# Optimization experiments

Hardware: AMD Instinct MI355X
Metric: run time of the kernel (lower is better)

The kernel has to match this reference:

```python
import jax, jax.numpy as jnp
import numpy as np

B, L, D, H = 4, 2048, 512, 8
HD = D // H  # 64
MAX_REL = 4


def setup_inputs() -> dict:
    key = jax.random.key(0)
    ks = jax.random.split(key, 13)
    s = 1.0 / np.sqrt(D)
    return {
        "q": jax.random.normal(ks[0], (B, L, D), jnp.float32),
        "k": jax.random.normal(ks[1], (B, L, D), jnp.float32),
        "v": jax.random.normal(ks[2], (B, L, D), jnp.float32),
        "Wq": jax.random.normal(ks[3], (D, D), jnp.float32) * s,
        "bq": jax.random.normal(ks[4], (D,), jnp.float32) * 0.01,
        "Wk": jax.random.normal(ks[5], (D, D), jnp.float32) * s,
        "bk": jax.random.normal(ks[6], (D,), jnp.float32) * 0.01,
        "Wv": jax.random.normal(ks[7], (D, D), jnp.float32) * s,
        "bv": jax.random.normal(ks[8], (D,), jnp.float32) * 0.01,
        "Wo": jax.random.normal(ks[9], (D, D), jnp.float32) * s,
        "bo": jax.random.normal(ks[10], (D,), jnp.float32) * 0.01,
        "rel_k_table": jax.random.normal(ks[11], (2 * MAX_REL + 1, HD), jnp.float32),
        "rel_v_table": jax.random.normal(ks[12], (2 * MAX_REL + 1, HD), jnp.float32),
    }


def _to_heads(x):
    # [B, L, D] -> [B, H, L, HD]
    b, l, d = x.shape
    return x.reshape(b, l, H, d // H).transpose(0, 2, 1, 3)


def reference(q, k, v, Wq, bq, Wk, bk, Wv, bv, Wo, bo, rel_k_table, rel_v_table):
    # NOTE: in the source, the relative-attention output is overwritten by the
    # plain SDPA call immediately after, so observable math = SDPA only.
    # rel_k_table / rel_v_table are dead parameters (zero gradient).
    relu = jax.nn.relu
    qh = _to_heads(relu(q @ Wq.T + bq))  # [B,H,L,HD]
    kh = _to_heads(relu(k @ Wk.T + bk))
    vh = _to_heads(relu(v @ Wv.T + bv))
    # scale by sqrt(d_key)=sqrt(512), matching the original (not sqrt(head_dim))
    scores = jnp.einsum("bhqd,bhkd->bhqk", qh, kh) / jnp.sqrt(jnp.float32(D))
    attn = jax.nn.softmax(scores, axis=-1)
    out = jnp.einsum("bhqk,bhkd->bhqd", attn, vh)  # [B,H,L,HD]
    out = out.transpose(0, 2, 1, 3).reshape(B, L, D)
    return relu(out @ Wo.T + bo)
```

## Files before the change

### kernel.cpp

```cpp
#include <hip/hip_runtime.h>
#include <hip/hip_bf16.h>

#define B_  4
#define L_  2048
#define D_  512
#define H_  8
#define HD_ 64
#define M_  (B_ * L_)

typedef __bf16 bf16;
typedef __attribute__((ext_vector_type(8)))  __bf16 bf16x8;
typedef __attribute__((ext_vector_type(4)))  __bf16 bf16x4;
typedef __attribute__((ext_vector_type(16))) float  f32x16;

__device__ __forceinline__ f32x16 mfma32(bf16x8 a, bf16x8 b, f32x16 c) {
    return __builtin_amdgcn_mfma_f32_32x32x16_bf16(a, b, c, 0, 0, 0);
}

__device__ __forceinline__ void pack_body(const float* __restrict__ src,
                                          bf16* __restrict__ dst, int R,
                                          int m0, int k0)
{
    __shared__ __align__(16) bf16 tile[64][76];
    const int t = threadIdx.x;
#pragma unroll
    for (int rep = 0; rep < 4; rep++) {
        const int idx = rep * 256 + t;
        const int r = idx >> 4, c4 = idx & 15;
        const float4 f = *(const float4*)(src + (size_t)(m0 + r) * 512 + k0 + c4 * 4);
        bf16x4 v; v[0] = (bf16)f.x; v[1] = (bf16)f.y; v[2] = (bf16)f.z; v[3] = (bf16)f.w;
        *(bf16x4*)(&tile[r][c4 * 4]) = v;
    }
    __syncthreads();
#pragma unroll
    for (int rep = 0; rep < 2; rep++) {
        const int s = rep * 256 + t;
        const int ml = s & 63, kpl = s >> 6;
        const bf16x4 lo = *(const bf16x4*)(&tile[ml][kpl * 8]);
        const bf16x4 hi4 = *(const bf16x4*)(&tile[ml][kpl * 8 + 4]);
        bf16x8 v;
#pragma unroll
        for (int e = 0; e < 4; e++) { v[e] = lo[e]; v[e + 4] = hi4[e]; }
        *(bf16x8*)(dst + ((size_t)(k0 / 8 + kpl) * R + m0 + ml) * 8) = v;
    }
}

__global__ __launch_bounds__(256) void pack_all(
    const float* __restrict__ q, const float* __restrict__ k,
    const float* __restrict__ v,
    const float* __restrict__ W0, const float* __restrict__ W1,
    const float* __restrict__ W2, const float* __restrict__ W3,
    bf16* __restrict__ Wp, bf16* __restrict__ P0, bf16* __restrict__ P1,
    bf16* __restrict__ P2)
{
    const int z = blockIdx.z;
    if (z < 4) {
        if (blockIdx.x >= 8) return;
        const float* src = z == 0 ? W0 : z == 1 ? W1 : z == 2 ? W2 : W3;
        pack_body(src, Wp + (size_t)z * 64 * 512 * 8, 512, blockIdx.x * 64, blockIdx.y * 64);
    } else {
        const float* src = z == 4 ? q : z == 5 ? k : v;
        bf16* dst = z == 4 ? P0 : z == 5 ? P1 : P2;
        pack_body(src, dst, M_, blockIdx.x * 64, blockIdx.y * 64);
    }
}

struct PJob {
    const bf16* X; const bf16* W; const float* bias; void* out;
    float postmul; int mode;
};

__global__ __launch_bounds__(256, 3) void proj_kernel(PJob j0, PJob j1, PJob j2)
{
    const PJob jb = (blockIdx.z == 0) ? j0 : (blockIdx.z == 1) ? j1 : j2;
    const int w    = threadIdx.x >> 6;
    const int lane = threadIdx.x & 63;
    const int l31  = lane & 31;
    const int hi   = lane >> 5;
    const int m0 = blockIdx.x * 128;
    const int n0 = blockIdx.y * 128;
    const int mh = w & 1;
    const int nh = w >> 1;

    __shared__ __align__(16) bf16 Ab[2][8][64][8];
    __shared__ __align__(16) bf16 Bb[2][8][64][8];

    f32x16 acc[2][2];
#pragma unroll
    for (int mi = 0; mi < 2; mi++)
#pragma unroll
        for (int ni = 0; ni < 2; ni++)
#pragma unroll
            for (int r = 0; r < 16; r++) acc[mi][ni][r] = 0.0f;

    auto ldA = [&](int f, int k0) -> bf16x8 {
        return *(const bf16x8*)(jb.X + ((size_t)((k0 >> 3) + (f >> 2) * 2 + hi) * M_
                                        + m0 + (f & 3) * 32 + l31) * 8);
    };
    auto ldB = [&](int f, int k0) -> bf16x8 {
        return *(const bf16x8*)(jb.W + ((size_t)((k0 >> 3) + (f >> 2) * 2 + hi) * 512
                                        + n0 + (f & 3) * 32 + l31) * 8);
    };

    bf16x8 rA[2][2], rB[2][2];
#pragma unroll
    for (int i = 0; i < 2; i++) { rA[0][i] = ldA(w * 2 + i, 0);  rB[0][i] = ldB(w * 2 + i, 0); }
#pragma unroll
    for (int i = 0; i < 2; i++) {
        *(bf16x8*)(&Ab[0][w * 2 + i][lane][0]) = rA[0][i];
        *(bf16x8*)(&Bb[0][w * 2 + i][lane][0]) = rB[0][i];
    }
#pragma unroll
    for (int i = 0; i < 2; i++) { rA[1][i] = ldA(w * 2 + i, 32); rB[1][i] = ldB(w * 2 + i, 32); }
#pragma unroll
    for (int i = 0; i < 2; i++) { rA[0][i] = ldA(w * 2 + i, 64); rB[0][i] = ldB(w * 2 + i, 64); }
    __syncthreads();

#pragma unroll
    for (int it = 0; it < 16; it++) {
        const int cur = it & 1;
#pragma unroll
        for (int ks = 0; ks < 2; ks++) {
            const bf16x8 a0 = *(const bf16x8*)(&Ab[cur][ks * 4 + mh * 2 + 0][lane][0]);
            const bf16x8 a1 = *(const bf16x8*)(&Ab[cur][ks * 4 + mh * 2 + 1][lane][0]);
            const bf16x8 b0 = *(const bf16x8*)(&Bb[cur][ks * 4 + nh * 2 + 0][lane][0]);
            const bf16x8 b1 = *(const bf16x8*)(&Bb[cur][ks * 4 + nh * 2 + 1][lane][0]);
            acc[0][0] = mfma32(a0, b0, acc[0][0]);
            acc[0][1] = mfma32(a0, b1, acc[0][1]);
            acc[1][0] = mfma32(a1, b0, acc[1][0]);
            acc[1][1] = mfma32(a1, b1, acc[1][1]);
        }
        if (it < 15) {
            const int s = (it + 1) & 1;
#pragma unroll
            for (int i = 0; i < 2; i++) {
                *(bf16x8*)(&Ab[1 - cur][w * 2 + i][lane][0]) = rA[s][i];
                *(bf16x8*)(&Bb[1 - cur][w * 2 + i][lane][0]) = rB[s][i];
            }
            if (it < 13) {
#pragma unroll
                for (int i = 0; i < 2; i++) {
                    rA[s][i] = ldA(w * 2 + i, (it + 3) * 32);
                    rB[s][i] = ldB(w * 2 + i, (it + 3) * 32);
                }
            }
            __syncthreads();
        }
    }

    const int mode = jb.mode;
#pragma unroll
    for (int ni = 0; ni < 2; ni++) {
        const int col = n0 + (nh * 2 + ni) * 32 + l31;
        const float bn = jb.bias[col];
#pragma unroll
        for (int mi = 0; mi < 2; mi++)
#pragma unroll
            for (int r = 0; r < 16; r++) {
                const int row = m0 + (mh * 2 + mi) * 32 + (r & 3) + 8 * (r >> 2) + 4 * hi;
                float v = fmaxf(acc[mi][ni][r] + bn, 0.0f);
                if (mode == 2) {
                    ((float*)jb.out)[(size_t)row * D_ + col] = v;
                } else {
                    v *= jb.postmul;
                    const int b = row >> 11, l = row & (L_ - 1);
                    const int h = col >> 6,  hd = col & (HD_ - 1);
                    const int bh = b * H_ + h;
                    size_t idx;
                    if (mode == 0) {
                        idx = ((size_t)bh * L_ + l) * HD_ + hd;
                    } else if (mode == 1) {
                        idx = (((size_t)bh * 8 + (hd >> 3)) * L_ + l) * 8 + (hd & 7);
                    } else {
                        const int swzl = (l & ~15) | (l & 3) | ((l & 4) << 1) | ((l & 8) >> 1);
                        idx = (((size_t)bh * 256 + (swzl >> 3)) * 64 + hd) * 8 + (swzl & 7);
                    }
                    ((bf16*)jb.out)[idx] = (bf16)v;
                }
            }
    }
}

__global__ __launch_bounds__(128, 2) void attn_kernel(
    const bf16* __restrict__ qh, const bf16* __restrict__ Kp,
    const bf16* __restrict__ Vp, bf16* __restrict__ Op)
{
    const int w    = threadIdx.x >> 6;
    const int lane = threadIdx.x & 63;
    const int l31  = lane & 31;
    const int hi   = lane >> 5;

    const int lin  = blockIdx.x + (blockIdx.y << 5);
    const int xcd  = lin & 7;
    const int slot = lin >> 3;
    const int bh   = (xcd << 2) + (slot >> 5);
    const int qb   = (slot & 31) * 64 + w * 32;

    const bf16* Q   = qh + (size_t)bh * L_ * HD_;
    const bf16* Kpb = Kp + (size_t)bh * 8 * L_ * 8;
    const bf16* Vpb = Vp + (size_t)bh * 256 * 64 * 8;

    __shared__ __align__(16) bf16 Vb[2][8][64][8];

    bf16x8 qf[4];
#pragma unroll
    for (int ks = 0; ks < 4; ks++)
        qf[ks] = *(const bf16x8*)(Q + (size_t)(qb + l31) * HD_ + ks * 16 + hi * 8);

    f32x16 zz;
#pragma unroll
    for (int r = 0; r < 16; r++) zz[r] = 0.0f;
    f32x16 o0 = zz, o1 = zz, lacc = zz;
    bf16x8 ones;
#pragma unroll
    for (int u = 0; u < 8; u++) ones[u] = (bf16)1.0f;

    auto ldK = [&](int f, int t) -> bf16x8 {
        return *(const bf16x8*)(Kpb + ((size_t)((f >> 1) * 2 + hi) * L_
                                       + t * 64 + (f & 1) * 32 + l31) * 8);
    };
    auto ldV = [&](int f, int t) -> bf16x8 {
        return *(const bf16x8*)(Vpb + ((size_t)(t * 8 + (f >> 1) * 2 + hi) * 64
                                       + (f & 1) * 32 + l31) * 8);
    };

    bf16x8 kr[8], vr[2][4];
#pragma unroll
    for (int i = 0; i < 4; i++) vr[0][i] = ldV(w * 4 + i, 0);
#pragma unroll
    for (int i = 0; i < 4; i++) *(bf16x8*)(&Vb[0][w * 4 + i][lane][0]) = vr[0][i];
#pragma unroll
    for (int i = 0; i < 4; i++) vr[1][i] = ldV(w * 4 + i, 1);
#pragma unroll
    for (int i = 0; i < 4; i++) vr[0][i] = ldV(w * 4 + i, 2);
#pragma unroll
    for (int f = 0; f < 8; f++) kr[f] = ldK(f, 0);
    __syncthreads();

    auto tile_body = [&](int t, int cur, int nxt) {
        f32x16 s0 = mfma32(kr[0], qf[0], zz);
        f32x16 s1 = mfma32(kr[1], qf[0], zz);
#pragma unroll
        for (int ks = 1; ks < 4; ks++) {
            s0 = mfma32(kr[ks * 2 + 0], qf[ks], s0);
            s1 = mfma32(kr[ks * 2 + 1], qf[ks], s1);
        }
        if (t < 31) {
#pragma unroll
            for (int f = 0; f < 8; f++) kr[f] = ldK(f, t + 1);
        }

#pragma unroll
        for (int r = 0; r < 16; r++) s0[r] = __builtin_amdgcn_exp2f(s0[r]);
        {
            bf16x8 pf0, pf1;
#pragma unroll
            for (int u = 0; u < 8; u++) { pf0[u] = (bf16)s0[u]; pf1[u] = (bf16)s0[8 + u]; }
            o0   = mfma32(pf0, *(const bf16x8*)(&Vb[cur][0][lane][0]), o0);
            o1   = mfma32(pf0, *(const bf16x8*)(&Vb[cur][1][lane][0]), o1);
            lacc = mfma32(pf0, ones, lacc);
            o0   = mfma32(pf1, *(const bf16x8*)(&Vb[cur][2][lane][0]), o0);
            o1   = mfma32(pf1, *(const bf16x8*)(&Vb[cur][3][lane][0]), o1);
            lacc = mfma32(pf1, ones, lacc);
        }
#pragma unroll
        for (int r = 0; r < 16; r++) s1[r] = __builtin_amdgcn_exp2f(s1[r]);
        {
            bf16x8 pf2, pf3;
#pragma unroll
            for (int u = 0; u < 8; u++) { pf2[u] = (bf16)s1[u]; pf3[u] = (bf16)s1[8 + u]; }
            o0   = mfma32(pf2, *(const bf16x8*)(&Vb[cur][4][lane][0]), o0);
            o1   = mfma32(pf2, *(const bf16x8*)(&Vb[cur][5][lane][0]), o1);
            lacc = mfma32(pf2, ones, lacc);
            o0   = mfma32(pf3, *(const bf16x8*)(&Vb[cur][6][lane][0]), o0);
            o1   = mfma32(pf3, *(const bf16x8*)(&Vb[cur][7][lane][0]), o1);
            lacc = mfma32(pf3, ones, lacc);
        }

        if (t < 31) {
#pragma unroll
            for (int i = 0; i < 4; i++)
                *(bf16x8*)(&Vb[1 - cur][w * 4 + i][lane][0]) = vr[nxt][i];
            const int tn = (t + 3 < 32) ? t + 3 : 31;
#pragma unroll
            for (int i = 0; i < 4; i++) vr[nxt][i] = ldV(w * 4 + i, tn);
            __syncthreads();
        }
    };

    for (int tt = 0; tt < 16; tt++) {
        tile_body(2 * tt + 0, 0, 1);
        tile_body(2 * tt + 1, 1, 0);
    }

    const int b = bh >> 3, h = bh & 7;
#pragma unroll
    for (int r = 0; r < 16; r++) {
        const int rl = (r & 3) + 8 * (r >> 2) + 4 * hi;
        const float inv = 1.0f / lacc[r];
        const int m = b * L_ + qb + rl;
        const int c0 = h * HD_ + l31;
        Op[((size_t)(c0 >> 3) * M_ + m) * 8 + (c0 & 7)] = (bf16)(o0[r] * inv);
        const int c1 = c0 + 32;
        Op[((size_t)(c1 >> 3) * M_ + m) * 8 + (c1 & 7)] = (bf16)(o1[r] * inv);
    }
}

extern "C" void kernel_launch(void* const* d_in, const int* in_sizes, int n_in,
                              void* d_out, int out_size, void* d_ws, size_t ws_size,
                              hipStream_t stream)
{
    (void)in_sizes; (void)n_in; (void)out_size;
    const float* q  = (const float*)d_in[0];
    const float* k  = (const float*)d_in[1];
    const float* v  = (const float*)d_in[2];
    const float* Wq = (const float*)d_in[3];
    const float* bq = (const float*)d_in[4];
    const float* Wk = (const float*)d_in[5];
    const float* bk = (const float*)d_in[6];
    const float* Wv = (const float*)d_in[7];
    const float* bv = (const float*)d_in[8];
    const float* Wo = (const float*)d_in[9];
    const float* bo = (const float*)d_in[10];
    float* out = (float*)d_out;

    char* ws = (char*)d_ws;
    const size_t MB = 1024 * 1024;
    bf16* P0  = (bf16*)(ws);
    bf16* P1  = (bf16*)(ws + 8 * MB);
    bf16* P2  = (bf16*)(ws + 16 * MB);
    bf16* Wp  = (bf16*)(ws + 24 * MB);
    bf16* qh  = (bf16*)(d_out);
    bf16* Kp  = (bf16*)((char*)d_out + 8 * MB);
    bf16* Opb = P1;

    bf16* Wqp = Wp;
    bf16* Wkp = Wp + (size_t)64 * 512 * 8;
    bf16* Wvp = Wp + (size_t)2 * 64 * 512 * 8;
    bf16* Wop = Wp + (size_t)3 * 64 * 512 * 8;

    const float SCALE_LOG2E = 0.06377946282349575f;

    dim3 pb(256);
    pack_all<<<dim3(128, 8, 7), pb, 0, stream>>>(q, k, v, Wq, Wk, Wv, Wo,
                                                 Wp, P0, P1, P2);

    if (ws_size >= (size_t)34 * MB) {
        bf16* VpN = (bf16*)(ws + 26 * MB);
        PJob jq{P0, Wqp, bq, qh,  SCALE_LOG2E, 0};
        PJob jk{P1, Wkp, bk, Kp,  1.0f, 1};
        PJob jv{P2, Wvp, bv, VpN, 1.0f, 3};
        proj_kernel<<<dim3(64, 4, 3), pb, 0, stream>>>(jq, jk, jv);

        attn_kernel<<<dim3(32, 32), dim3(128), 0, stream>>>(qh, Kp, VpN, Opb);
    } else {
        bf16* Vp = P0;
        PJob jq{P0, Wqp, bq, qh, SCALE_LOG2E, 0};
        PJob jk{P1, Wkp, bk, Kp, 1.0f, 1};
        proj_kernel<<<dim3(64, 4, 2), pb, 0, stream>>>(jq, jk, jk);

        PJob jv{P2, Wvp, bv, Vp, 1.0f, 3};
        proj_kernel<<<dim3(64, 4, 1), pb, 0, stream>>>(jv, jv, jv);

        attn_kernel<<<dim3(32, 32), dim3(128), 0, stream>>>(qh, Kp, Vp, Opb);
    }

    PJob jo{Opb, Wop, bo, out, 1.0f, 2};
    proj_kernel<<<dim3(64, 4, 1), pb, 0, stream>>>(jo, jo, jo);
}
```

Baseline: 197.0 us.

## Fuse fp32-to-bf16 activation conversion into QKV projection GEMM loads

Removes the separate packing pass for q/k/v and has the QKV projection kernel load fp32 activations directly, converting to bf16 while staging into shared memory. Weight packing stays as a small separate kernel. This eliminates a full write and re-read of the packed activations and drops the workspace-size branch. In exchange the GEMM loads twice as many bytes per A tile and uses more registers for the fp32 staging buffers, which could lower occupancy or add LDS bank conflicts.

```diff
diff --git a/kernel.cpp b/kernel.cpp
--- a/kernel.cpp
+++ b/kernel.cpp
@@ -45,34 +45,24 @@
     }
 }
 
-__global__ __launch_bounds__(256) void pack_all(
-    const float* __restrict__ q, const float* __restrict__ k,
-    const float* __restrict__ v,
+__global__ __launch_bounds__(256) void pack_w(
     const float* __restrict__ W0, const float* __restrict__ W1,
     const float* __restrict__ W2, const float* __restrict__ W3,
-    bf16* __restrict__ Wp, bf16* __restrict__ P0, bf16* __restrict__ P1,
-    bf16* __restrict__ P2)
+    bf16* __restrict__ Wp)
 {
     const int z = blockIdx.z;
-    if (z < 4) {
-        if (blockIdx.x >= 8) return;
-        const float* src = z == 0 ? W0 : z == 1 ? W1 : z == 2 ? W2 : W3;
-        pack_body(src, Wp + (size_t)z * 64 * 512 * 8, 512, blockIdx.x * 64, blockIdx.y * 64);
-    } else {
-        const float* src = z == 4 ? q : z == 5 ? k : v;
-        bf16* dst = z == 4 ? P0 : z == 5 ? P1 : P2;
-        pack_body(src, dst, M_, blockIdx.x * 64, blockIdx.y * 64);
-    }
+    const float* src = z == 0 ? W0 : z == 1 ? W1 : z == 2 ? W2 : W3;
+    pack_body(src, Wp + (size_t)z * 64 * 512 * 8, 512, blockIdx.x * 64, blockIdx.y * 64);
 }
 
 struct PJob {
-    const bf16* X; const bf16* W; const float* bias; void* out;
-    float postmul; int mode;
+    const bf16* X; const float* Xf; const bf16* W; const float* bias;
+    void* out; float postmul; int mode;
 };
 
-__global__ __launch_bounds__(256, 3) void proj_kernel(PJob j0, PJob j1, PJob j2)
-{
-    const PJob jb = (blockIdx.z == 0) ? j0 : (blockIdx.z == 1) ? j1 : j2;
+template<bool FP32A>
+__device__ __forceinline__ void proj_body(const PJob jb)
+{
     const int w    = threadIdx.x >> 6;
     const int lane = threadIdx.x & 63;
     const int l31  = lane & 31;
@@ -103,17 +93,52 @@
     };
 
     bf16x8 rA[2][2], rB[2][2];
-#pragma unroll
-    for (int i = 0; i < 2; i++) { rA[0][i] = ldA(w * 2 + i, 0);  rB[0][i] = ldB(w * 2 + i, 0); }
-#pragma unroll
-    for (int i = 0; i < 2; i++) {
-        *(bf16x8*)(&Ab[0][w * 2 + i][lane][0]) = rA[0][i];
+    float4 rT[2][4];
+
+    auto ldT = [&](int s, int k0) {
+#pragma unroll
+        for (int rep = 0; rep < 4; rep++) {
+            const int idx = rep * 256 + (int)threadIdx.x;
+            rT[s][rep] = *(const float4*)(jb.Xf + (size_t)(m0 + (idx >> 3)) * 512
+                                          + k0 + (idx & 7) * 4);
+        }
+    };
+    auto stA = [&](int s, int buf) {
+#pragma unroll
+        for (int rep = 0; rep < 4; rep++) {
+            const int idx = rep * 256 + (int)threadIdx.x;
+            const int r = idx >> 3, c4 = idx & 7;
+            const float4 f = rT[s][rep];
+            bf16x4 v; v[0] = (bf16)f.x; v[1] = (bf16)f.y;
+            v[2] = (bf16)f.z; v[3] = (bf16)f.w;
+            const int fs = ((c4 >> 2) << 2) | (r >> 5);
+            const int ln = (r & 31) | (((c4 >> 1) & 1) << 5);
+            *(bf16x4*)(&Ab[buf][fs][ln][(c4 & 1) * 4]) = v;
+        }
+    };
+
+    if constexpr (FP32A) {
+        ldT(0, 0); stA(0, 0); ldT(1, 32); ldT(0, 64);
+    } else {
+#pragma unroll
+        for (int i = 0; i < 2; i++) rA[0][i] = ldA(w * 2 + i, 0);
+#pragma unroll
+        for (int i = 0; i < 2; i++)
+            *(bf16x8*)(&Ab[0][w * 2 + i][lane][0]) = rA[0][i];
+#pragma unroll
+        for (int i = 0; i < 2; i++) rA[1][i] = ldA(w * 2 + i, 32);
+#pragma unroll
+        for (int i = 0; i < 2; i++) rA[0][i] = ldA(w * 2 + i, 64);
+    }
+#pragma unroll
+    for (int i = 0; i < 2; i++) rB[0][i] = ldB(w * 2 + i, 0);
+#pragma unroll
+    for (int i = 0; i < 2; i++)
         *(bf16x8*)(&Bb[0][w * 2 + i][lane][0]) = rB[0][i];
-    }
-#pragma unroll
-    for (int i = 0; i < 2; i++) { rA[1][i] = ldA(w * 2 + i, 32); rB[1][i] = ldB(w * 2 + i, 32); }
-#pragma unroll
-    for (int i = 0; i < 2; i++) { rA[0][i] = ldA(w * 2 + i, 64); rB[0][i] = ldB(w * 2 + i, 64); }
+#pragma unroll
+    for (int i = 0; i < 2; i++) rB[1][i] = ldB(w * 2 + i, 32);
+#pragma unroll
+    for (int i = 0; i < 2; i++) rB[0][i] = ldB(w * 2 + i, 64);
     __syncthreads();
 
 #pragma unroll
@@ -132,17 +157,27 @@
         }
         if (it < 15) {
             const int s = (it + 1) & 1;
-#pragma unroll
-            for (int i = 0; i < 2; i++) {
-                *(bf16x8*)(&Ab[1 - cur][w * 2 + i][lane][0]) = rA[s][i];
+            if constexpr (FP32A) {
+                stA(s, 1 - cur);
+            } else {
+#pragma unroll
+                for (int i = 0; i < 2; i++)
+                    *(bf16x8*)(&Ab[1 - cur][w * 2 + i][lane][0]) = rA[s][i];
+            }
+#pragma unroll
+            for (int i = 0; i < 2; i++)
                 *(bf16x8*)(&Bb[1 - cur][w * 2 + i][lane][0]) = rB[s][i];
-            }
             if (it < 13) {
-#pragma unroll
-                for (int i = 0; i < 2; i++) {
-                    rA[s][i] = ldA(w * 2 + i, (it + 3) * 32);
+                if constexpr (FP32A) {
+                    ldT(s, (it + 3) * 32);
+                } else {
+#pragma unroll
+                    for (int i = 0; i < 2; i++)
+                        rA[s][i] = ldA(w * 2 + i, (it + 3) * 32);
+                }
+#pragma unroll
+                for (int i = 0; i < 2; i++)
                     rB[s][i] = ldB(w * 2 + i, (it + 3) * 32);
-                }
             }
             __syncthreads();
         }
@@ -181,6 +216,18 @@
     }
 }
 
+__global__ __launch_bounds__(256, 3) void proj_kernel(PJob j0, PJob j1, PJob j2)
+{
+    const PJob jb = (blockIdx.z == 0) ? j0 : (blockIdx.z == 1) ? j1 : j2;
+    proj_body<false>(jb);
+}
+
+__global__ __launch_bounds__(256, 3) void proj_qkv_kernel(PJob j0, PJob j1, PJob j2)
+{
+    const PJob jb = (blockIdx.z == 0) ? j0 : (blockIdx.z == 1) ? j1 : j2;
+    proj_body<true>(jb);
+}
+
 __global__ __launch_bounds__(128, 2) void attn_kernel(
     const bf16* __restrict__ qh, const bf16* __restrict__ Kp,
     const bf16* __restrict__ Vp, bf16* __restrict__ Op)
@@ -310,7 +357,7 @@
                               void* d_out, int out_size, void* d_ws, size_t ws_size,
                               hipStream_t stream)
 {
-    (void)in_sizes; (void)n_in; (void)out_size;
+    (void)in_sizes; (void)n_in; (void)out_size; (void)ws_size;
     const float* q  = (const float*)d_in[0];
     const float* k  = (const float*)d_in[1];
     const float* v  = (const float*)d_in[2];
@@ -326,13 +373,11 @@
 
     char* ws = (char*)d_ws;
     const size_t MB = 1024 * 1024;
-    bf16* P0  = (bf16*)(ws);
-    bf16* P1  = (bf16*)(ws + 8 * MB);
-    bf16* P2  = (bf16*)(ws + 16 * MB);
-    bf16* Wp  = (bf16*)(ws + 24 * MB);
+    bf16* Vp  = (bf16*)(ws);
+    bf16* Opb = (bf16*)(ws + 8 * MB);
+    bf16* Wp  = (bf16*)(ws + 16 * MB);
     bf16* qh  = (bf16*)(d_out);
     bf16* Kp  = (bf16*)((char*)d_out + 8 * MB);
-    bf16* Opb = P1;
 
     bf16* Wqp = Wp;
     bf16* Wkp = Wp + (size_t)64 * 512 * 8;
@@ -341,30 +386,15 @@
 
     const float SCALE_LOG2E = 0.06377946282349575f;
 
-    dim3 pb(256);
-    pack_all<<<dim3(128, 8, 7), pb, 0, stream>>>(q, k, v, Wq, Wk, Wv, Wo,
-                                                 Wp, P0, P1, P2);
-
-    if (ws_size >= (size_t)34 * MB) {
-        bf16* VpN = (bf16*)(ws + 26 * MB);
-        PJob jq{P0, Wqp, bq, qh,  SCALE_LOG2E, 0};
-        PJob jk{P1, Wkp, bk, Kp,  1.0f, 1};
-        PJob jv{P2, Wvp, bv, VpN, 1.0f, 3};
-        proj_kernel<<<dim3(64, 4, 3), pb, 0, stream>>>(jq, jk, jv);
-
-        attn_kernel<<<dim3(32, 32), dim3(128), 0, stream>>>(qh, Kp, VpN, Opb);
-    } else {
-        bf16* Vp = P0;
-        PJob jq{P0, Wqp, bq, qh, SCALE_LOG2E, 0};
-        PJob jk{P1, Wkp, bk, Kp, 1.0f, 1};
-        proj_kernel<<<dim3(64, 4, 2), pb, 0, stream>>>(jq, jk, jk);
-
-        PJob jv{P2, Wvp, bv, Vp, 1.0f, 3};
-        proj_kernel<<<dim3(64, 4, 1), pb, 0, stream>>>(jv, jv, jv);
-
-        attn_kernel<<<dim3(32, 32), dim3(128), 0, stream>>>(qh, Kp, Vp, Opb);
-    }
-
-    PJob jo{Opb, Wop, bo, out, 1.0f, 2};
-    proj_kernel<<<dim3(64, 4, 1), pb, 0, stream>>>(jo, jo, jo);
-}
+    pack_w<<<dim3(8, 8, 4), dim3(256), 0, stream>>>(Wq, Wk, Wv, Wo, Wp);
+
+    PJob jq{nullptr, q, Wqp, bq, qh, SCALE_LOG2E, 0};
+    PJob jk{nullptr, k, Wkp, bk, Kp, 1.0f, 1};
+    PJob jv{nullptr, v, Wvp, bv, Vp, 1.0f, 3};
+    proj_qkv_kernel<<<dim3(64, 4, 3), dim3(256), 0, stream>>>(jq, jk, jv);
+
+    attn_kernel<<<dim3(32, 32), dim3(128), 0, stream>>>(qh, Kp, Vp, Opb);
+
+    PJob jo{Opb, nullptr, Wop, bo, out, 1.0f, 2};
+    proj_kernel<<<dim3(64, 4, 1), dim3(256), 0, stream>>>(jo, jo, jo);
+}
```

After: 192.7 us. -2.2%, faster.
